# Kernel tuning notes

Measured on AMD Instinct MI355X. Metric: run time of the kernel, lower is better.

## Reference

```python
import jax, jax.numpy as jnp
import numpy as np

B, N, D = 32, 4096, 128
H = D // 2      # GRU hidden = 64
Q = D // 4      # MLP hidden = 32
HORIZON = 28


def setup_inputs() -> dict:
    key = jax.random.key(0)
    ks = jax.random.split(key, 16)
    s = lambda k, shape, fan: jax.random.normal(k, shape, jnp.float32) * (1.0 / np.sqrt(fan))
    return {
        "features": jax.random.normal(ks[0], (B, N, D), jnp.float32),
        "last_value": jax.random.uniform(ks[1], (B, N), jnp.float32),
        # GRU (input_size=1, hidden=H), PyTorch gate order r,z,n
        "W_ih": s(ks[2], (3 * H, 1), 1),
        "W_hh": s(ks[3], (3 * H, H), H),
        "b_ih": s(ks[4], (3 * H,), H),
        "b_hh": s(ks[5], (3 * H,), H),
        # hidden_proj: Linear(D -> H)
        "Wp": s(ks[6], (H, D), D), "bp": s(ks[7], (H,), D),
        # output_proj: Linear(H->Q), ReLU, Linear(Q->1)
        "Wo1": s(ks[8], (Q, H), H), "bo1": s(ks[9], (Q,), H),
        "Wo2": s(ks[10], (1, Q), Q), "bo2": s(ks[11], (1,), Q),
        # refine_gate: Linear(D->Q), ReLU, Linear(Q->horizon), Sigmoid
        "Wg1": s(ks[12], (Q, D), D), "bg1": s(ks[13], (Q,), D),
        "Wg2": s(ks[14], (HORIZON, Q), Q), "bg2": s(ks[15], (HORIZON,), Q),
        "log_decay": jnp.asarray(-2.3, jnp.float32),
    }


def reference(features, last_value, W_ih, W_hh, b_ih, b_hh, Wp, bp,
              Wo1, bo1, Wo2, bo2, Wg1, bg1, Wg2, bg2, log_decay):
    b, n, d = features.shape
    h0 = features.reshape(b * n, d) @ Wp.T + bp          # [BN, H]
    x0 = last_value.reshape(b * n, 1)                    # [BN, 1]

    def step(carry, _):
        h, x = carry
        gi = x @ W_ih.T + b_ih                           # [BN, 3H]
        gh = h @ W_hh.T + b_hh                           # [BN, 3H]
        r = jax.nn.sigmoid(gi[:, :H] + gh[:, :H])
        z = jax.nn.sigmoid(gi[:, H:2 * H] + gh[:, H:2 * H])
        ncell = jnp.tanh(gi[:, 2 * H:] + r * gh[:, 2 * H:])
        h_new = (1.0 - z) * ncell + z * h
        pred = jax.nn.relu(h_new @ Wo1.T + bo1) @ Wo2.T + bo2  # [BN, 1] (dropout = eval)
        return (h_new, pred), pred[:, 0]

    (_, _), preds = jax.lax.scan(step, (h0, x0), None, length=HORIZON)
    gru_pred = preds.T.reshape(b, n, HORIZON)            # [B, N, horizon]

    gate = jax.nn.sigmoid(jax.nn.relu(features @ Wg1.T + bg1) @ Wg2.T + bg2)
    t = jnp.arange(1, HORIZON + 1, dtype=jnp.float32)
    decay_curve = jnp.exp(-jnp.exp(log_decay) * t)       # [horizon]
    decay_pred = last_value[..., None] * decay_curve
    return gate * gru_pred + (1.0 - gate) * decay_pred
```

## Files before the change

### kernel.cpp

```cpp
#include <hip/hip_runtime.h>

#define TPB 256
#define HOR 28
#define LOG2E 1.44269504088896340736f

typedef _Float16 f16;
typedef __attribute__((ext_vector_type(2))) _Float16 f16x2;
typedef __attribute__((ext_vector_type(4))) _Float16 f16x4;
typedef __attribute__((ext_vector_type(8))) _Float16 f16x8;
typedef __attribute__((ext_vector_type(4))) float f32x4;

union V8 { f16x8 v8; f16x4 v4[2]; f16x2 h2[4]; };

#define MFMA16(A,B,C) __builtin_amdgcn_mfma_f32_16x16x32_f16((A),(B),(C),0,0,0)

__device__ __forceinline__ f16x2 pk2(float a, float b) {
    return __builtin_bit_cast(f16x2, __builtin_amdgcn_cvt_pkrtz(a, b));
}

__global__ __launch_bounds__(TPB, 2) void predictor_kernel(
    const float* __restrict__ features,
    const float* __restrict__ last_value,
    const float* __restrict__ W_ih,
    const float* __restrict__ W_hh,
    const float* __restrict__ b_ih,
    const float* __restrict__ b_hh,
    const float* __restrict__ Wp,
    const float* __restrict__ bp,
    const float* __restrict__ Wo1,
    const float* __restrict__ bo1,
    const float* __restrict__ Wo2,
    const float* __restrict__ bo2,
    const float* __restrict__ Wg1,
    const float* __restrict__ bg1,
    const float* __restrict__ Wg2,
    const float* __restrict__ bg2,
    const float* __restrict__ log_decay,
    float* __restrict__ out)
{
    __shared__ __align__(16) f16 s_mem[16128];

    const int tid = threadIdx.x;
    const int wv = tid >> 6, ln = tid & 63;
    const int a = ln & 15, g = ln >> 4;
    const int row0 = blockIdx.x * 64 + wv * 16;

    const f32x4 ZF = {0.f, 0.f, 0.f, 0.f};

    f16* s_wp  = s_mem;
    f16* s_wg1 = s_mem + 8704;
    f16* s_wg2 = s_mem + 13056;

    for (int i = tid; i < 64 * 128; i += TPB) s_wp [(i >> 7) * 136 + (i & 127)] = (f16)Wp[i];
    for (int i = tid; i < 32 * 128; i += TPB) s_wg1[(i >> 7) * 136 + (i & 127)] = (f16)Wg1[i];
    for (int i = tid; i < 32 * 32; i += TPB) {
        int t = i >> 5, s = i & 31;
        int q = ((s >> 2) & 1) * 16 + ((s >> 3) & 3) * 4 + (s & 3);
        s_wg2[t * 40 + s] = (f16)((t < HOR) ? Wg2[t * 32 + q] : 0.0f);
    }

    f16x2 wR[4][2], wZ[4][2], wN[4][2], bR[4][2], bZ[4][2], bN[4][2], bH[4][2];
    #pragma unroll
    for (int c = 0; c < 4; ++c) {
        #pragma unroll
        for (int p = 0; p < 2; ++p) {
            int u0 = c * 16 + g * 4 + 2 * p, u1 = u0 + 1;
            wR[c][p] = pk2(W_ih[u0] * -LOG2E, W_ih[u1] * -LOG2E);
            wZ[c][p] = pk2(W_ih[64 + u0] * -LOG2E, W_ih[64 + u1] * -LOG2E);
            wN[c][p] = pk2(W_ih[128 + u0] * 2.0f * LOG2E, W_ih[128 + u1] * 2.0f * LOG2E);
            bR[c][p] = pk2((b_ih[u0] + b_hh[u0]) * -LOG2E, (b_ih[u1] + b_hh[u1]) * -LOG2E);
            bZ[c][p] = pk2((b_ih[64 + u0] + b_hh[64 + u0]) * -LOG2E,
                           (b_ih[64 + u1] + b_hh[64 + u1]) * -LOG2E);
            bN[c][p] = pk2(b_ih[128 + u0] * 2.0f * LOG2E, b_ih[128 + u1] * 2.0f * LOG2E);
            bH[c][p] = pk2(b_hh[128 + u0] * 2.0f * LOG2E, b_hh[128 + u1] * 2.0f * LOG2E);
        }
    }
    f16x2 bo1q[2][2], wo2q[2][2];
    #pragma unroll
    for (int mt = 0; mt < 2; ++mt)
        #pragma unroll
        for (int p = 0; p < 2; ++p) {
            int q0 = mt * 16 + g * 4 + 2 * p;
            bo1q[mt][p] = pk2(bo1[q0], bo1[q0 + 1]);
            wo2q[mt][p] = pk2(Wo2[q0], Wo2[q0 + 1]);
        }
    const float bo2v = bo2[0];
    const float edc  = LOG2E * __builtin_amdgcn_exp2f(LOG2E * log_decay[0]);
    const float lv   = last_value[row0 + a];

    V8 FF[4];
    #pragma unroll
    for (int kt = 0; kt < 4; ++kt) {
        const float* fp = features + (size_t)(row0 + a) * 128 + kt * 32 + g * 8;
        f32x4 v0 = *(const f32x4*)fp;
        f32x4 v1 = *(const f32x4*)(fp + 4);
        FF[kt].h2[0] = pk2(v0[0], v0[1]); FF[kt].h2[1] = pk2(v0[2], v0[3]);
        FF[kt].h2[2] = pk2(v1[0], v1[1]); FF[kt].h2[3] = pk2(v1[2], v1[3]);
    }

    __syncthreads();

    f32x4 h4[4];
    {
        f16x2 bpq[4][2];
        #pragma unroll
        for (int c = 0; c < 4; ++c)
            #pragma unroll
            for (int p = 0; p < 2; ++p) {
                int u0 = c * 16 + g * 4 + 2 * p;
                bpq[c][p] = pk2(bp[u0], bp[u0 + 1]);
            }
        #pragma unroll
        for (int nt = 0; nt < 4; ++nt) {
            f32x4 acc = ZF;
            #pragma unroll
            for (int kt = 0; kt < 4; ++kt) {
                f16x8 w = *(const f16x8*)&s_wp[(nt * 16 + a) * 136 + kt * 32 + g * 8];
                acc = MFMA16(w, FF[kt].v8, acc);
            }
            #pragma unroll
            for (int r = 0; r < 4; ++r) acc[r] += (float)bpq[nt][r >> 1][r & 1];
            h4[nt] = acc;
        }
    }

    float gA0, gA1, gA2, gA3, gB0, gB1, gB2, gB3;
    {
        f32x4 a1acc[2];
        #pragma unroll
        for (int mt = 0; mt < 2; ++mt) {
            f32x4 acc = ZF;
            #pragma unroll
            for (int kt = 0; kt < 4; ++kt) {
                f16x8 w = *(const f16x8*)&s_wg1[(mt * 16 + a) * 136 + kt * 32 + g * 8];
                acc = MFMA16(w, FF[kt].v8, acc);
            }
            #pragma unroll
            for (int r = 0; r < 4; ++r) {
                int q0 = mt * 16 + g * 4 + r;
                acc[r] = fmaxf(acc[r] + bg1[q0], 0.f);
            }
            a1acc[mt] = acc;
        }
        V8 A1;
        A1.h2[0] = pk2(a1acc[0][0], a1acc[0][1]);
        A1.h2[1] = pk2(a1acc[0][2], a1acc[0][3]);
        A1.h2[2] = pk2(a1acc[1][0], a1acc[1][1]);
        A1.h2[3] = pk2(a1acc[1][2], a1acc[1][3]);
        float gv[2][4];
        #pragma unroll
        for (int mt = 0; mt < 2; ++mt) {
            f32x4 acc = ZF;
            f16x8 w = *(const f16x8*)&s_wg2[(mt * 16 + a) * 40 + g * 8];
            acc = MFMA16(w, A1.v8, acc);
            #pragma unroll
            for (int r = 0; r < 4; ++r) {
                int t0 = mt * 16 + g * 4 + r;
                float lg = acc[r] + ((t0 < HOR) ? bg2[t0] : 0.f);
                gv[mt][r] = __builtin_amdgcn_rcpf(1.0f + __builtin_amdgcn_exp2f(-LOG2E * lg));
            }
        }
        gA0 = gv[0][0]; gA1 = gv[0][1]; gA2 = gv[0][2]; gA3 = gv[0][3];
        gB0 = gv[1][0]; gB1 = gv[1][1]; gB2 = gv[1][2]; gB3 = gv[1][3];
    }

    __syncthreads();
    f16* s_whh = s_mem;
    f16* s_wo1 = s_mem + 13824;
    for (int i = tid; i < 192 * 64; i += TPB) {
        int r = i >> 6, c = i & 63;
        float s = (r < 128) ? -LOG2E : 2.0f * LOG2E;
        s_whh[r * 72 + c] = (f16)(W_hh[i] * s);
    }
    for (int i = tid; i < 32 * 64; i += TPB) s_wo1[(i >> 6) * 72 + (i & 63)] = (f16)Wo1[i];
    __syncthreads();

    V8 WgR[4][2], WgZ[4][2], WgN[4][2];
    #pragma unroll
    for (int c = 0; c < 4; ++c) {
        #pragma unroll
        for (int kt = 0; kt < 2; ++kt) {
            int rowR = (c * 16 + a) * 72 + kt * 32 + 4 * g;
            int rowZ = (64 + c * 16 + a) * 72 + kt * 32 + 4 * g;
            int rowN = (128 + c * 16 + a) * 72 + kt * 32 + 4 * g;
            WgR[c][kt].v4[0] = *(const f16x4*)&s_whh[rowR];
            WgR[c][kt].v4[1] = *(const f16x4*)&s_whh[rowR + 16];
            WgZ[c][kt].v4[0] = *(const f16x4*)&s_whh[rowZ];
            WgZ[c][kt].v4[1] = *(const f16x4*)&s_whh[rowZ + 16];
            WgN[c][kt].v4[0] = *(const f16x4*)&s_whh[rowN];
            WgN[c][kt].v4[1] = *(const f16x4*)&s_whh[rowN + 16];
        }
    }

    V8 F0, F1;
    F0.h2[0] = pk2(h4[0][0], h4[0][1]); F0.h2[1] = pk2(h4[0][2], h4[0][3]);
    F0.h2[2] = pk2(h4[1][0], h4[1][1]); F0.h2[3] = pk2(h4[1][2], h4[1][3]);
    F1.h2[0] = pk2(h4[2][0], h4[2][1]); F1.h2[1] = pk2(h4[2][2], h4[2][3]);
    F1.h2[2] = pk2(h4[3][0], h4[3][1]); F1.h2[3] = pk2(h4[3][2], h4[3][3]);

    float x = lv;

#define GATE_MMA(ACC, WARR, c) do { \
        ACC = MFMA16(WARR[c][0].v8, F0.v8, ZF); \
        ACC = MFMA16(WARR[c][1].v8, F1.v8, ACC); } while (0)

#define GRU_CELL(c, AR, AZ, AN) do { \
        _Pragma("unroll") \
        for (int p = 0; p < 2; ++p) { \
            f16x2 afR = x2 * wR[c][p] + bR[c][p]; \
            f16x2 afZ = x2 * wZ[c][p] + bZ[c][p]; \
            f16x2 afN = x2 * wN[c][p] + bN[c][p]; \
            _Pragma("unroll") \
            for (int q = 0; q < 2; ++q) { \
                int r = p * 2 + q; \
                float ar = AR[r] + (float)afR[q]; \
                float rg = __builtin_amdgcn_rcpf(1.0f + __builtin_amdgcn_exp2f(ar)); \
                float az = AZ[r] + (float)afZ[q]; \
                float pb = 1.0f + __builtin_amdgcn_exp2f(az); \
                float ghn = AN[r] + (float)bH[c][p][q]; \
                float E  = __builtin_amdgcn_exp2f(fmaf(rg, ghn, (float)afN[q])); \
                float pE = 1.0f + E; \
                float rD = __builtin_amdgcn_rcpf(pb * pE); \
                float zg = rD * pE; \
                float ivE = rD * pb; \
                float nc = fmaf(-2.0f, ivE, 1.0f); \
                float hv = h4[c][r]; \
                h4[c][r] = fmaf(zg, hv - nc, nc); \
            } \
        } } while (0)

    #pragma unroll 1
    for (int t = 0; t < HOR; ++t) {
        f16x2 x2 = pk2(x, x);
        f32x4 aR0, aZ0, aN0, aR1, aZ1, aN1;
        GATE_MMA(aR0, WgR, 0); GATE_MMA(aZ0, WgZ, 0); GATE_MMA(aN0, WgN, 0);
        GATE_MMA(aR1, WgR, 1); GATE_MMA(aZ1, WgZ, 1); GATE_MMA(aN1, WgN, 1);
        GRU_CELL(0, aR0, aZ0, aN0);
        GRU_CELL(1, aR1, aZ1, aN1);
        GATE_MMA(aR0, WgR, 2); GATE_MMA(aZ0, WgZ, 2); GATE_MMA(aN0, WgN, 2);
        GATE_MMA(aR1, WgR, 3); GATE_MMA(aZ1, WgZ, 3); GATE_MMA(aN1, WgN, 3);
        GRU_CELL(2, aR0, aZ0, aN0);
        GRU_CELL(3, aR1, aZ1, aN1);

        F0.h2[0] = pk2(h4[0][0], h4[0][1]); F0.h2[1] = pk2(h4[0][2], h4[0][3]);
        F0.h2[2] = pk2(h4[1][0], h4[1][1]); F0.h2[3] = pk2(h4[1][2], h4[1][3]);
        F1.h2[0] = pk2(h4[2][0], h4[2][1]); F1.h2[1] = pk2(h4[2][2], h4[2][3]);
        F1.h2[2] = pk2(h4[3][0], h4[3][1]); F1.h2[3] = pk2(h4[3][2], h4[3][3]);

        V8 wo;
        f32x4 o0 = ZF, o1 = ZF;
        wo.v4[0] = *(const f16x4*)&s_wo1[a * 72 + 4 * g];
        wo.v4[1] = *(const f16x4*)&s_wo1[a * 72 + 16 + 4 * g];
        o0 = MFMA16(wo.v8, F0.v8, o0);
        wo.v4[0] = *(const f16x4*)&s_wo1[a * 72 + 32 + 4 * g];
        wo.v4[1] = *(const f16x4*)&s_wo1[a * 72 + 48 + 4 * g];
        o0 = MFMA16(wo.v8, F1.v8, o0);
        wo.v4[0] = *(const f16x4*)&s_wo1[(16 + a) * 72 + 4 * g];
        wo.v4[1] = *(const f16x4*)&s_wo1[(16 + a) * 72 + 16 + 4 * g];
        o1 = MFMA16(wo.v8, F0.v8, o1);
        wo.v4[0] = *(const f16x4*)&s_wo1[(16 + a) * 72 + 32 + 4 * g];
        wo.v4[1] = *(const f16x4*)&s_wo1[(16 + a) * 72 + 48 + 4 * g];
        o1 = MFMA16(wo.v8, F1.v8, o1);

        float part = 0.f;
        #pragma unroll
        for (int p = 0; p < 2; ++p)
            #pragma unroll
            for (int q = 0; q < 2; ++q) {
                int r = 2 * p + q;
                part += fmaxf(o0[r] + (float)bo1q[0][p][q], 0.f) * (float)wo2q[0][p][q];
                part += fmaxf(o1[r] + (float)bo1q[1][p][q], 0.f) * (float)wo2q[1][p][q];
            }
        part += __shfl_xor(part, 16);
        part += __shfl_xor(part, 32);
        float pred = part + bo2v;

        if (g == ((t >> 2) & 3)) {
            float s01 = (t & 1) ? ((t & 16) ? gB1 : gA1) : ((t & 16) ? gB0 : gA0);
            float s23 = (t & 1) ? ((t & 16) ? gB3 : gA3) : ((t & 16) ? gB2 : gA2);
            float gvf = (t & 2) ? s23 : s01;
            float dc = __builtin_amdgcn_exp2f(-edc * (float)(t + 1));
            float lvdc = lv * dc;
            out[(size_t)(row0 + a) * HOR + t] = fmaf(gvf, pred - lvdc, lvdc);
        }
        x = pred;
    }
#undef GATE_MMA
#undef GRU_CELL
}

extern "C" void kernel_launch(void* const* d_in, const int* in_sizes, int n_in,
                              void* d_out, int out_size, void* d_ws, size_t ws_size,
                              hipStream_t stream) {
    const float* features   = (const float*)d_in[0];
    const float* last_value = (const float*)d_in[1];
    const float* W_ih       = (const float*)d_in[2];
    const float* W_hh       = (const float*)d_in[3];
    const float* b_ih       = (const float*)d_in[4];
    const float* b_hh       = (const float*)d_in[5];
    const float* Wp         = (const float*)d_in[6];
    const float* bp         = (const float*)d_in[7];
    const float* Wo1        = (const float*)d_in[8];
    const float* bo1        = (const float*)d_in[9];
    const float* Wo2        = (const float*)d_in[10];
    const float* bo2        = (const float*)d_in[11];
    const float* Wg1        = (const float*)d_in[12];
    const float* bg1        = (const float*)d_in[13];
    const float* Wg2        = (const float*)d_in[14];
    const float* bg2        = (const float*)d_in[15];
    const float* log_decay  = (const float*)d_in[16];
    float* out = (float*)d_out;

    dim3 grid(131072 / 64), block(TPB);
    predictor_kernel<<<grid, block, 0, stream>>>(
        features, last_value, W_ih, W_hh, b_ih, b_hh, Wp, bp,
        Wo1, bo1, Wo2, bo2, Wg1, bg1, Wg2, bg2, log_decay, out);
}
```

Before: 243.8 us.

## Stream GRU recurrent weights from LDS each step to raise occupancy

Stops holding the 96-VGPR W_hh MFMA fragments in registers across the time loop and instead reloads them from shared memory inside each gate matmul. Launch bounds go from 2 to 3 blocks per CU so the freed registers buy more resident waves. An empty asm memory barrier keeps the compiler from hoisting the LDS loads out of the loop. The cost is extra LDS traffic and load latency in the recurrent critical path, in exchange for more latency hiding from higher occupancy.

```diff
diff --git a/kernel.cpp b/kernel.cpp
--- a/kernel.cpp
+++ b/kernel.cpp
@@ -18,7 +18,7 @@
     return __builtin_bit_cast(f16x2, __builtin_amdgcn_cvt_pkrtz(a, b));
 }
 
-__global__ __launch_bounds__(TPB, 2) void predictor_kernel(
+__global__ __launch_bounds__(TPB, 3) void predictor_kernel(
     const float* __restrict__ features,
     const float* __restrict__ last_value,
     const float* __restrict__ W_ih,
@@ -175,22 +175,7 @@
     for (int i = tid; i < 32 * 64; i += TPB) s_wo1[(i >> 6) * 72 + (i & 63)] = (f16)Wo1[i];
     __syncthreads();
 
-    V8 WgR[4][2], WgZ[4][2], WgN[4][2];
-    #pragma unroll
-    for (int c = 0; c < 4; ++c) {
-        #pragma unroll
-        for (int kt = 0; kt < 2; ++kt) {
-            int rowR = (c * 16 + a) * 72 + kt * 32 + 4 * g;
-            int rowZ = (64 + c * 16 + a) * 72 + kt * 32 + 4 * g;
-            int rowN = (128 + c * 16 + a) * 72 + kt * 32 + 4 * g;
-            WgR[c][kt].v4[0] = *(const f16x4*)&s_whh[rowR];
-            WgR[c][kt].v4[1] = *(const f16x4*)&s_whh[rowR + 16];
-            WgZ[c][kt].v4[0] = *(const f16x4*)&s_whh[rowZ];
-            WgZ[c][kt].v4[1] = *(const f16x4*)&s_whh[rowZ + 16];
-            WgN[c][kt].v4[0] = *(const f16x4*)&s_whh[rowN];
-            WgN[c][kt].v4[1] = *(const f16x4*)&s_whh[rowN + 16];
-        }
-    }
+    const int wr = a * 72 + 4 * g;
 
     V8 F0, F1;
     F0.h2[0] = pk2(h4[0][0], h4[0][1]); F0.h2[1] = pk2(h4[0][2], h4[0][3]);
@@ -200,9 +185,14 @@
 
     float x = lv;
 
-#define GATE_MMA(ACC, WARR, c) do { \
-        ACC = MFMA16(WARR[c][0].v8, F0.v8, ZF); \
-        ACC = MFMA16(WARR[c][1].v8, F1.v8, ACC); } while (0)
+#define GATE_MMA(ACC, BR, c) do { \
+        V8 w0_, w1_; \
+        w0_.v4[0] = *(const f16x4*)&s_whh[(BR + c * 16) * 72      + wr]; \
+        w0_.v4[1] = *(const f16x4*)&s_whh[(BR + c * 16) * 72 + 16 + wr]; \
+        w1_.v4[0] = *(const f16x4*)&s_whh[(BR + c * 16) * 72 + 32 + wr]; \
+        w1_.v4[1] = *(const f16x4*)&s_whh[(BR + c * 16) * 72 + 48 + wr]; \
+        ACC = MFMA16(w0_.v8, F0.v8, ZF); \
+        ACC = MFMA16(w1_.v8, F1.v8, ACC); } while (0)
 
 #define GRU_CELL(c, AR, AZ, AN) do { \
         _Pragma("unroll") \
@@ -231,14 +221,15 @@
 
     #pragma unroll 1
     for (int t = 0; t < HOR; ++t) {
+        asm volatile("" ::: "memory");
         f16x2 x2 = pk2(x, x);
         f32x4 aR0, aZ0, aN0, aR1, aZ1, aN1;
-        GATE_MMA(aR0, WgR, 0); GATE_MMA(aZ0, WgZ, 0); GATE_MMA(aN0, WgN, 0);
-        GATE_MMA(aR1, WgR, 1); GATE_MMA(aZ1, WgZ, 1); GATE_MMA(aN1, WgN, 1);
+        GATE_MMA(aR0, 0, 0); GATE_MMA(aZ0, 64, 0); GATE_MMA(aN0, 128, 0);
+        GATE_MMA(aR1, 0, 1); GATE_MMA(aZ1, 64, 1); GATE_MMA(aN1, 128, 1);
         GRU_CELL(0, aR0, aZ0, aN0);
         GRU_CELL(1, aR1, aZ1, aN1);
-        GATE_MMA(aR0, WgR, 2); GATE_MMA(aZ0, WgZ, 2); GATE_MMA(aN0, WgN, 2);
-        GATE_MMA(aR1, WgR, 3); GATE_MMA(aZ1, WgZ, 3); GATE_MMA(aN1, WgN, 3);
+        GATE_MMA(aR0, 0, 2); GATE_MMA(aZ0, 64, 2); GATE_MMA(aN0, 128, 2);
+        GATE_MMA(aR1, 0, 3); GATE_MMA(aZ1, 64, 3); GATE_MMA(aN1, 128, 3);
         GRU_CELL(2, aR0, aZ0, aN0);
         GRU_CELL(3, aR1, aZ1, aN1);
 
@@ -249,17 +240,17 @@
 
         V8 wo;
         f32x4 o0 = ZF, o1 = ZF;
-        wo.v4[0] = *(const f16x4*)&s_wo1[a * 72 + 4 * g];
-        wo.v4[1] = *(const f16x4*)&s_wo1[a * 72 + 16 + 4 * g];
+        wo.v4[0] = *(const f16x4*)&s_wo1[wr];
+        wo.v4[1] = *(const f16x4*)&s_wo1[wr + 16];
         o0 = MFMA16(wo.v8, F0.v8, o0);
-        wo.v4[0] = *(const f16x4*)&s_wo1[a * 72 + 32 + 4 * g];
-        wo.v4[1] = *(const f16x4*)&s_wo1[a * 72 + 48 + 4 * g];
+        wo.v4[0] = *(const f16x4*)&s_wo1[wr + 32];
+        wo.v4[1] = *(const f16x4*)&s_wo1[wr + 48];
         o0 = MFMA16(wo.v8, F1.v8, o0);
-        wo.v4[0] = *(const f16x4*)&s_wo1[(16 + a) * 72 + 4 * g];
-        wo.v4[1] = *(const f16x4*)&s_wo1[(16 + a) * 72 + 16 + 4 * g];
+        wo.v4[0] = *(const f16x4*)&s_wo1[16 * 72 + wr];
+        wo.v4[1] = *(const f16x4*)&s_wo1[16 * 72 + wr + 16];
         o1 = MFMA16(wo.v8, F0.v8, o1);
-        wo.v4[0] = *(const f16x4*)&s_wo1[(16 + a) * 72 + 32 + 4 * g];
-        wo.v4[1] = *(const f16x4*)&s_wo1[(16 + a) * 72 + 48 + 4 * g];
+        wo.v4[0] = *(const f16x4*)&s_wo1[16 * 72 + wr + 32];
+        wo.v4[1] = *(const f16x4*)&s_wo1[16 * 72 + wr + 48];
         o1 = MFMA16(wo.v8, F1.v8, o1);
 
         float part = 0.f;
```

Result: slower. 276.8 us (+13.5%).
